# Kernel optimization log

Hardware: AMD Instinct MI355X
Metric: run time of the kernel (lower is better)

The kernel has to match this reference:

```python
import jax, jax.numpy as jnp
import numpy as np

B, S = 32, 128
NUM_Q, NUM_C = 10000, 256
DIM_K, DIM_E, DIM_CORRECT = 128, 128, 50


def setup_inputs() -> dict:
    key = jax.random.key(0)
    ks = jax.random.split(key, 16)
    w = lambda k, shape: jax.random.normal(k, shape, dtype=jnp.float32) * 0.05
    z = lambda n: jnp.zeros((n,), jnp.float32)
    # q_matrix: sparse binary concept-question map with small smoothing (typical LPKT gamma)
    q_matrix = (jax.random.uniform(ks[4], (NUM_Q + 10, NUM_C)) < 0.03).astype(jnp.float32) + 0.03
    return {
        'e_data': jax.random.randint(ks[0], (B, S), 0, NUM_Q),
        'at_data': jax.random.randint(ks[1], (B, S), 0, 3600),
        'it_data': jax.random.randint(ks[2], (B, S), 0, 43200),
        'a_data': jax.random.uniform(ks[3], (B, S), dtype=jnp.float32),
        'q_matrix': q_matrix,
        'e_E': w(ks[5], (NUM_Q + 10, DIM_K)),
        'at_E': w(ks[6], (3610, DIM_K)),
        'it_E': w(ks[7], (43210, DIM_K)),
        'W1': w(ks[8], (DIM_E + DIM_K + DIM_CORRECT, DIM_K)), 'b1': z(DIM_K),
        'W2': w(ks[9], (4 * DIM_K, DIM_K)), 'b2': z(DIM_K),
        'W3': w(ks[10], (4 * DIM_K, DIM_K)), 'b3': z(DIM_K),
        'W4': w(ks[11], (3 * DIM_K, DIM_K)), 'b4': z(DIM_K),
        'W5': w(ks[12], (DIM_E + DIM_K, DIM_K)), 'b5': z(DIM_K),
        'h0': w(ks[13], (NUM_C, DIM_K)),
    }


def reference(e_data, at_data, it_data, a_data, q_matrix, e_E, at_E, it_E,
              W1, b1, W2, b2, W3, b3, W4, b4, W5, b5, h0):
    Bn, Sn = e_data.shape
    K = W1.shape[1]
    e_emb = e_E[e_data]          # [B,S,K]
    at_emb = at_E[at_data]       # [B,S,K]
    it_emb = it_E[it_data]       # [B,S,K]
    a_rep = jnp.broadcast_to(a_data[:, :, None], (Bn, Sn, DIM_CORRECT))
    all_learning = jnp.concatenate([e_emb, at_emb, a_rep], -1) @ W1 + b1  # [B,S,K]
    q_all = q_matrix[e_data]     # [B,S,C]

    h_init = jnp.broadcast_to(h0, (Bn,) + h0.shape)              # [B,C,K]
    h_tilde_init = jnp.einsum('bc,bck->bk', q_all[:, 0], h_init)  # [B,K]
    learning_init = jnp.zeros((Bn, K), all_learning.dtype)

    xs = jax.tree.map(lambda x: jnp.swapaxes(x, 0, 1),
                      (q_all[:, :-1], q_all[:, 1:], all_learning[:, :-1],
                       it_emb[:, :-1], e_emb[:, 1:]))

    def step(carry, x):
        h, h_tilde, learning_pre = carry
        q_e, q_next, learning, it, e_next = x
        zcat = jnp.concatenate([learning_pre, it, learning, h_tilde], -1)  # [B,4K]
        lg = jnp.tanh(zcat @ W2 + b2)
        gamma_l = jax.nn.sigmoid(zcat @ W3 + b3)
        LG = gamma_l * (lg + 1.0) * 0.5                                    # [B,K]
        LG_tilde = q_e[:, :, None] * LG[:, None, :]                        # [B,C,K] (dropout=eval identity)
        gf_in = jnp.concatenate([h,
                                 jnp.broadcast_to(LG[:, None, :], h.shape),
                                 jnp.broadcast_to(it[:, None, :], h.shape)], -1)
        gamma_f = jax.nn.sigmoid(gf_in @ W4 + b4)                          # [B,C,K]
        h_new = LG_tilde + gamma_f * h
        h_tilde_new = jnp.einsum('bc,bck->bk', q_next, h_new)             # [B,K]
        y = jax.nn.sigmoid(jnp.concatenate([e_next, h_tilde_new], -1) @ W5 + b5).sum(-1) / K
        return (h_new, h_tilde_new, learning), y

    _, ys = jax.lax.scan(step, (h_init, h_tilde_init, learning_init), xs)  # ys: [S-1,B]
    pred = jnp.concatenate([jnp.zeros((Bn, 1), ys.dtype), ys.T], axis=1)    # [B,S]
    return pred
```

## Files before the change

### kernel.cpp

```cpp
#include <hip/hip_runtime.h>
#include <stdint.h>

#define S   128
#define NB  32
#define NC  256
#define DK  128
#define NSL 4
#define HROW 264

typedef __bf16 bf16x8 __attribute__((ext_vector_type(8)));
typedef float  f32x16 __attribute__((ext_vector_type(16)));
typedef unsigned int u32x4 __attribute__((ext_vector_type(4)));
typedef unsigned int u32x2 __attribute__((ext_vector_type(2)));
typedef _Float16 f16x2 __attribute__((ext_vector_type(2)));
static_assert(sizeof(bf16x8) == 16, "bf16x8 size");
static_assert(sizeof(f16x2) == 4, "f16x2 size");

#define OFF_AL   0
#define OFF_HT   OFF_AL
#define OFF_P2   524288
#define OFF_P3   1044480
#define OFF_PS   1564672
#define OFF_PY   2084864
#define OFF_WT5  2654208
#define OFF_CM   2670592

__device__ __forceinline__ float v_exp2(float x){ float r; asm("v_exp_f32 %0, %1" : "=v"(r) : "v"(x)); return r; }
__device__ __forceinline__ float v_rcp (float x){ float r; asm("v_rcp_f32 %0, %1" : "=v"(r) : "v"(x)); return r; }
__device__ __forceinline__ float sigm(float x){ return v_rcp(1.0f + v_exp2(x * -1.4426950408889634f)); }
__device__ __forceinline__ uint32_t pkbf(float lo, float hi){
  uint32_t r; asm("v_cvt_pk_bf16_f32 %0, %1, %2" : "=v"(r) : "v"(lo), "v"(hi)); return r;
}
__device__ __forceinline__ float bfhi(uint32_t w){ return __builtin_bit_cast(float, w & 0xffff0000u); }
__device__ __forceinline__ uint32_t pkh(float a, float b){
  return __builtin_bit_cast(uint32_t, __builtin_amdgcn_cvt_pkrtz(a, b));
}
__device__ __forceinline__ float fdot2u(uint32_t a, uint32_t b, float c){
  return __builtin_amdgcn_fdot2(__builtin_bit_cast(f16x2, a), __builtin_bit_cast(f16x2, b), c, false);
}
#define NLOG2E (-1.4426950408889634f)

__global__ __launch_bounds__(512) void k0_al(
    const int* __restrict__ e_data, const int* __restrict__ at_data,
    const float* __restrict__ a_data, const float* __restrict__ e_E,
    const float* __restrict__ at_E, const float* __restrict__ W1,
    const float* __restrict__ b1, float* __restrict__ ws)
{
  __shared__ float ein[32][128];
  __shared__ float atin[32][128];
  int b = blockIdx.x >> 2, q4 = blockIdx.x & 3, t0 = q4 * 32;
  for (int idx = threadIdx.x; idx < 32 * 128; idx += 512) {
    int r = idx >> 7, j = idx & 127;
    int ev  = e_data [b * S + t0 + r];
    int atv = at_data[b * S + t0 + r];
    ein [r][j] = e_E [ev  * DK + j];
    atin[r][j] = at_E[atv * DK + j];
  }
  __syncthreads();
  int j = threadIdx.x & 127, tq = threadIdx.x >> 7;
  float w1s = 0.f;
  for (int d = 0; d < 50; ++d) w1s += W1[(256 + d) * DK + j];
  float acc[8];
#pragma unroll
  for (int u = 0; u < 8; ++u) {
    int t = t0 + tq * 8 + u;
    acc[u] = b1[j] + a_data[b * S + t] * w1s;
  }
  for (int k = 0; k < 128; ++k) {
    float w = W1[k * DK + j];
#pragma unroll
    for (int u = 0; u < 8; ++u) acc[u] += ein[tq * 8 + u][k] * w;
  }
  for (int k = 0; k < 128; ++k) {
    float w = W1[(128 + k) * DK + j];
#pragma unroll
    for (int u = 0; u < 8; ++u) acc[u] += atin[tq * 8 + u][k] * w;
  }
#pragma unroll
  for (int u = 0; u < 8; ++u)
    ws[OFF_AL + (b * S + t0 + tq * 8 + u) * DK + j] = acc[u];
}

__global__ __launch_bounds__(256) void kT_tr(const float* __restrict__ W5, float* __restrict__ ws)
{
  int idx = blockIdx.x * 256 + threadIdx.x;
  int j = idx >> 7, k = idx & 127;
  ws[OFF_WT5 + j * DK + k] = W5[(128 + k) * DK + j];
}

__global__ __launch_bounds__(512) void k1_pre(
    const int* __restrict__ e_data, const int* __restrict__ it_data,
    const float* __restrict__ it_E, const float* __restrict__ e_E,
    const float* __restrict__ W2, const float* __restrict__ b2,
    const float* __restrict__ W3, const float* __restrict__ b3,
    const float* __restrict__ W4, const float* __restrict__ b4,
    const float* __restrict__ W5, const float* __restrict__ b5,
    float* __restrict__ ws)
{
  __shared__ float als[33][128];
  __shared__ float its[32][128];
  __shared__ float ens[32][128];
  int b = blockIdx.x >> 2, sh = blockIdx.x & 3, s0 = sh * 32;
  for (int idx = threadIdx.x; idx < 33 * 128; idx += 512) {
    int r = idx >> 7, j = idx & 127;
    int srow = s0 - 1 + r;
    als[r][j] = (srow >= 0) ? ws[OFF_AL + (b * S + srow) * DK + j] : 0.f;
  }
  for (int idx = threadIdx.x; idx < 32 * 128; idx += 512) {
    int r = idx >> 7, j = idx & 127;
    int itv = it_data[b * S + s0 + r];
    its[r][j] = it_E[itv * DK + j];
    int sg = s0 + r + 1; if (sg > 127) sg = 127;
    int ev = e_data[b * S + sg];
    ens[r][j] = e_E[ev * DK + j];
  }
  __syncthreads();
  int j = threadIdx.x & 127, sq = threadIdx.x >> 7;
  float p2[8], p3[8], pS[8], pY[8];
#pragma unroll
  for (int u = 0; u < 8; ++u) { p2[u] = b2[j]; p3[u] = b3[j]; pS[u] = b4[j]; pY[u] = b5[j]; }
  for (int k = 0; k < 128; ++k) {
    float w2 = W2[k * DK + j], w3 = W3[k * DK + j];
#pragma unroll
    for (int u = 0; u < 8; ++u) { float v = als[sq * 8 + u][k]; p2[u] += v * w2; p3[u] += v * w3; }
  }
  for (int k = 0; k < 128; ++k) {
    float w2 = W2[(128 + k) * DK + j], w3 = W3[(128 + k) * DK + j], w4 = W4[(256 + k) * DK + j];
#pragma unroll
    for (int u = 0; u < 8; ++u) { float v = its[sq * 8 + u][k]; p2[u] += v * w2; p3[u] += v * w3; pS[u] += v * w4; }
  }
  for (int k = 0; k < 128; ++k) {
    float w2 = W2[(256 + k) * DK + j], w3 = W3[(256 + k) * DK + j];
#pragma unroll
    for (int u = 0; u < 8; ++u) { float v = als[sq * 8 + u + 1][k]; p2[u] += v * w2; p3[u] += v * w3; }
  }
  for (int k = 0; k < 128; ++k) {
    float w5 = W5[k * DK + j];
#pragma unroll
    for (int u = 0; u < 8; ++u) pY[u] += ens[sq * 8 + u][k] * w5;
  }
#pragma unroll
  for (int u = 0; u < 8; ++u) {
    int s = s0 + sq * 8 + u;
    if (s < 127) {
      int o = (b * 127 + s) * DK + j;
      ws[OFF_P2 + o] = p2[u]; ws[OFF_P3 + o] = p3[u];
      ws[OFF_PS + o] = pS[u]; ws[OFF_PY + o] = pY[u];
    }
  }
}

__global__ __launch_bounds__(512, 2) void kmain(
    const int* __restrict__ e_data, const float* __restrict__ qmat,
    const float* __restrict__ W2, const float* __restrict__ W3,
    const float* __restrict__ W4, const float* __restrict__ h0,
    float* ws)
{
  __shared__ char     hsb[64 * HROW];
  __shared__ u32x4    W4B[4][8][64];
  __shared__ uint32_t W4Lh[64][128];
  __shared__ float    qbuf[3][64];
  __shared__ float    PST[2][3][128];
  __shared__ uint32_t htldp[64];
  __shared__ uint32_t LGp[64];

  const int bx = blockIdx.x;
  const int b = bx & 31, slice = bx >> 5;
  const int tid = threadIdx.x;
  const int lane = tid & 63, wv = tid >> 6;
  const int ct = wv >> 2, jt = wv & 3;
  const int lo = lane & 31, hi = lane >> 5;
  const int jA = tid >> 2, am = (tid >> 1) & 1, akh = tid & 1;
  const int jloc = jt * 32 + lo;

  uint32_t* cm32 = (uint32_t*)(ws + OFF_CM) + (size_t)b * 2048;

  uint32_t Awh[32];
  {
    const float* Wm = am ? W3 : W2;
#pragma unroll
    for (int i = 0; i < 32; ++i) {
      float w0 = Wm[(384 + akh * 64 + 2 * i) * DK + jA];
      float w1 = Wm[(384 + akh * 64 + 2 * i + 1) * DK + jA];
      Awh[i] = pkh(w0, w1);
    }
  }
  float hm[16];
#pragma unroll
  for (int r = 0; r < 16; ++r) {
    int cl = ct * 32 + (r & 3) + 8 * (r >> 2) + 4 * hi;
    hm[r] = h0[(slice * 64 + cl) * DK + jloc];
  }

  {
    uint32_t* w4b = (uint32_t*)&W4B[0][0][0];
#pragma unroll
    for (int it = 0; it < 16; ++it) {
      int idx = tid + it * 512;
      int w = idx & 3, l = (idx >> 2) & 63, kk = (idx >> 8) & 7, jb = idx >> 11;
      int llo = l & 31, lhi = l >> 5;
      int row = kk * 16 + lhi * 8 + 2 * w, col = jb * 32 + llo;
      w4b[idx] = pkbf(W4[row * DK + col], W4[(row + 1) * DK + col]);
    }
  }
#pragma unroll
  for (int it = 0; it < 16; ++it) {
    int idx = tid + it * 512, kp = idx >> 7, jj = idx & 127;
    W4Lh[kp][jj] = pkh(W4[(128 + 2 * kp) * DK + jj], W4[(128 + 2 * kp + 1) * DK + jj]);
  }
  if (tid < 64) {
    qbuf[0][tid] = qmat[e_data[b * S + 0] * NC + slice * 64 + tid];
    qbuf[1][tid] = qmat[e_data[b * S + 1] * NC + slice * 64 + tid];
  }
  if (tid < 384) {
    int mm = tid >> 7, jj = tid & 127;
    int off = (mm == 0) ? OFF_P2 : (mm == 1) ? OFF_P3 : OFF_PS;
    PST[0][mm][jj] = ws[off + (b * 127 + 0) * DK + jj];
  }
#pragma unroll
  for (int r = 0; r < 16; ++r) {
    int cl = ct * 32 + (r & 3) + 8 * (r >> 2) + 4 * hi;
    *(uint16_t*)(hsb + cl * HROW + jloc * 2) = (uint16_t)pkbf(hm[r], 0.f);
  }
  __syncthreads();

  {
    float ht = 0.f;
#pragma unroll
    for (int r = 0; r < 16; ++r) {
      int cl = ct * 32 + (r & 3) + 8 * (r >> 2) + 4 * hi;
      ht += qbuf[0][cl] * hm[r];
    }
    ht += __shfl_xor(ht, 32);
    if (hi == 0)
      __hip_atomic_store(&cm32[1 * 1024 + (slice * 2 + ct) * 128 + jloc],
                         pkbf(0.f, ht) | 1u, __ATOMIC_RELAXED, __HIP_MEMORY_SCOPE_AGENT);
  }

  float v0 = 0.f, v1 = 0.f;

#pragma unroll 1
  for (int s = 0; s < S - 1; ++s) {
    const int par = s & 1;

    float qld = 0.f, pld = 0.f;
    if (tid >= 448)
      qld = qmat[e_data[b * S + min(s + 2, S - 1)] * NC + slice * 64 + (tid - 448)];
    if (tid >= 128) {
      int mm = (tid - 128) >> 7, jj = tid & 127;
      int off = (mm == 0) ? OFF_P2 : (mm == 1) ? OFF_P3 : OFF_PS;
      pld = ws[off + (b * 127 + min(s + 1, 126)) * DK + jj];
    }

    f32x16 acc;
#pragma unroll
    for (int r = 0; r < 16; ++r) acc[r] = 0.f;
    {
      const char* base = hsb + (ct * 32 + lo) * HROW;
#pragma unroll
      for (int kk = 0; kk < 8; ++kk) {
        u32x2 a0 = *(const u32x2*)(base + kk * 32 + hi * 16);
        u32x2 a1 = *(const u32x2*)(base + kk * 32 + hi * 16 + 8);
        u32x4 af4; af4[0] = a0[0]; af4[1] = a0[1]; af4[2] = a1[0]; af4[3] = a1[1];
        u32x4 bfr = W4B[jt][kk][lane];
        acc = __builtin_amdgcn_mfma_f32_32x32x16_bf16(
            __builtin_bit_cast(bf16x8, af4), __builtin_bit_cast(bf16x8, bfr), acc, 0, 0, 0);
      }
    }

    if (wv == 0) {
      const uint32_t tgt = (uint32_t)(s + 1);
      const uint32_t* src = cm32 + ((s + 1) & 1) * 1024;
      uint32_t g[16];
      for (;;) {
        uint32_t tsum = 0;
#pragma unroll
        for (int i = 0; i < 16; ++i) {
          g[i] = __hip_atomic_load(&src[(i >> 1) * 128 + (i & 1) * 64 + lane],
                                   __ATOMIC_RELAXED, __HIP_MEMORY_SCOPE_AGENT);
          tsum += g[i] & 0xffffu;
        }
        if (__all(tsum == 16u * tgt)) break;
        __builtin_amdgcn_s_sleep(1);
      }
      v0 = 0.f; v1 = 0.f;
#pragma unroll
      for (int i = 0; i < 16; i += 2) { v0 += bfhi(g[i]); v1 += bfhi(g[i + 1]); }
      float vn0 = __shfl_xor(v0, 1), vn1 = __shfl_xor(v1, 1);
      if (!(lane & 1)) {
        htldp[lane >> 1]        = pkh(v0, vn0);
        htldp[32 + (lane >> 1)] = pkh(v1, vn1);
      }
    }
    __syncthreads();

    if (slice == 0 && s > 0 && wv == 0) {
      ws[OFF_HT + (b * 127 + (s - 1)) * DK + lane]      = v0;
      ws[OFF_HT + (b * 127 + (s - 1)) * DK + 64 + lane] = v1;
    }
    {
      float p = 0.f;
#pragma unroll
      for (int t = 0; t < 32; ++t)
        p = fdot2u(htldp[akh * 32 + t], Awh[t], p);
      p += __shfl_xor(p, 1);
      float po = __shfl_xor(p, 2);
      float v2 = am ? po : p;
      float v3 = am ? p : po;
      v2 += PST[par][0][jA];
      v3 += PST[par][1][jA];
      float lg = sigm(v3) * sigm(2.f * v2);
      float lgn = __shfl_xor(lg, 4);
      if ((tid & 7) == 0) LGp[tid >> 3] = pkh(lg, lgn);
    }
    __syncthreads();

    if (tid >= 448) qbuf[(s + 2) % 3][tid - 448] = qld;
    if (tid >= 128) {
      int mm = (tid - 128) >> 7, jj = tid & 127;
      PST[(s + 1) & 1][mm][jj] = pld;
    }
    {
      float pB = 0.f;
#pragma unroll
      for (int t = 0; t < 32; ++t)
        pB = fdot2u(LGp[hi * 32 + t], W4Lh[hi * 32 + t][jloc], pB);
      pB += __shfl_xor(pB, 32);
      float sb = PST[par][2][jloc] + pB;
      float sn = sb * NLOG2E;
      f16x2 l2 = __builtin_bit_cast(f16x2, LGp[jloc >> 1]);
      float lgj = (float)l2[jloc & 1];
      const float* qc = &qbuf[s % 3][0];
      const float* qn = &qbuf[(s + 1) % 3][0];
      float ht = 0.f;
#pragma unroll
      for (int q4 = 0; q4 < 4; ++q4) {
        int cbase = ct * 32 + 8 * q4 + 4 * hi;
        float4 qe4 = *(const float4*)&qc[cbase];
        float4 qn4 = *(const float4*)&qn[cbase];
#pragma unroll
        for (int rr = 0; rr < 4; ++rr) {
          int r = 4 * q4 + rr;
          float qe = (rr == 0) ? qe4.x : (rr == 1) ? qe4.y : (rr == 2) ? qe4.z : qe4.w;
          float qq = (rr == 0) ? qn4.x : (rr == 1) ? qn4.y : (rr == 2) ? qn4.z : qn4.w;
          int cl = cbase + rr;
          float g = v_rcp(1.0f + v_exp2(fmaf(acc[r], NLOG2E, sn)));
          float hn = fmaf(g, hm[r], qe * lgj);
          hm[r] = hn; ht = fmaf(qq, hn, ht);
          *(uint16_t*)(hsb + cl * HROW + jloc * 2) = (uint16_t)pkbf(hn, 0.f);
        }
      }
      ht += __shfl_xor(ht, 32);
      if (hi == 0)
        __hip_atomic_store(&cm32[(s & 1) * 1024 + (slice * 2 + ct) * 128 + jloc],
                           pkbf(0.f, ht) | (uint32_t)(s + 2),
                           __ATOMIC_RELAXED, __HIP_MEMORY_SCOPE_AGENT);
    }
    __syncthreads();
  }

  if (slice == 0 && wv == 0) {
    const uint32_t* src = cm32 + 0 * 1024;
    uint32_t g[16];
    for (;;) {
      uint32_t tsum = 0;
#pragma unroll
      for (int i = 0; i < 16; ++i) {
        g[i] = __hip_atomic_load(&src[(i >> 1) * 128 + (i & 1) * 64 + lane],
                                 __ATOMIC_RELAXED, __HIP_MEMORY_SCOPE_AGENT);
        tsum += g[i] & 0xffffu;
      }
      if (__all(tsum == 16u * 128u)) break;
      __builtin_amdgcn_s_sleep(1);
    }
    float t0 = 0.f, t1 = 0.f;
#pragma unroll
    for (int i = 0; i < 16; i += 2) { t0 += bfhi(g[i]); t1 += bfhi(g[i + 1]); }
    ws[OFF_HT + (b * 127 + 126) * DK + lane]      = t0;
    ws[OFF_HT + (b * 127 + 126) * DK + 64 + lane] = t1;
  }
}

__global__ __launch_bounds__(128) void k2_y(const float* __restrict__ ws, float* __restrict__ out)
{
  __shared__ float hts[8][128];
  __shared__ float part[2][8];
  int b = blockIdx.x >> 4, ch = blockIdx.x & 15, s0 = ch * 8;
  int j = threadIdx.x;
#pragma unroll
  for (int u = 0; u < 8; ++u) {
    int s = s0 + u;
    hts[u][j] = (s < 127) ? ws[OFF_HT + (b * 127 + s) * DK + j] : 0.f;
  }
  __syncthreads();
  float acc[8];
#pragma unroll
  for (int u = 0; u < 8; ++u) {
    int s = s0 + u;
    acc[u] = (s < 127) ? ws[OFF_PY + (b * 127 + s) * DK + j] : 0.f;
  }
  const float4* w5 = (const float4*)(ws + OFF_WT5 + j * DK);
#pragma unroll 8
  for (int i = 0; i < 32; ++i) {
    float4 w = w5[i];
#pragma unroll
    for (int u = 0; u < 8; ++u) {
      float4 h4 = *(const float4*)&hts[u][4 * i];
      acc[u] += w.x * h4.x + w.y * h4.y + w.z * h4.z + w.w * h4.w;
    }
  }
#pragma unroll
  for (int u = 0; u < 8; ++u) {
    float v = sigm(acc[u]);
#pragma unroll
    for (int off = 32; off >= 1; off >>= 1) v += __shfl_xor(v, off);
    if ((j & 63) == 0) part[j >> 6][u] = v;
  }
  __syncthreads();
  if (j < 8) {
    int s = s0 + j;
    if (s < 127) out[b * S + s + 1] = (part[0][j] + part[1][j]) * (1.0f / 128.0f);
  }
  if (j == 0 && ch == 0) out[b * S] = 0.f;
}

extern "C" void kernel_launch(void* const* d_in, const int* in_sizes, int n_in,
                              void* d_out, int out_size, void* d_ws, size_t ws_size,
                              hipStream_t stream)
{
  (void)in_sizes; (void)n_in; (void)out_size; (void)ws_size;
  const int*   e_data  = (const int*)  d_in[0];
  const int*   at_data = (const int*)  d_in[1];
  const int*   it_data = (const int*)  d_in[2];
  const float* a_data  = (const float*)d_in[3];
  const float* qmat    = (const float*)d_in[4];
  const float* e_E     = (const float*)d_in[5];
  const float* at_E    = (const float*)d_in[6];
  const float* it_E    = (const float*)d_in[7];
  const float* W1 = (const float*)d_in[8];  const float* b1 = (const float*)d_in[9];
  const float* W2 = (const float*)d_in[10]; const float* b2 = (const float*)d_in[11];
  const float* W3 = (const float*)d_in[12]; const float* b3 = (const float*)d_in[13];
  const float* W4 = (const float*)d_in[14]; const float* b4 = (const float*)d_in[15];
  const float* W5 = (const float*)d_in[16]; const float* b5 = (const float*)d_in[17];
  const float* h0 = (const float*)d_in[18];
  float* ws  = (float*)d_ws;
  float* out = (float*)d_out;

  hipMemsetAsync((char*)d_ws + (size_t)OFF_CM * 4, 0, (size_t)NB * 2 * 8 * 128 * 4, stream);

  k0_al <<<128, 512, 0, stream>>>(e_data, at_data, a_data, e_E, at_E, W1, b1, ws);
  kT_tr <<<64, 256, 0, stream>>>(W5, ws);
  k1_pre<<<128, 512, 0, stream>>>(e_data, it_data, it_E, e_E, W2, b2, W3, b3, W4, b4, W5, b5, ws);
  kmain <<<128, 512, 0, stream>>>(e_data, qmat, W2, W3, W4, h0, ws);
  k2_y  <<<512, 128, 0, stream>>>(ws, out);
}
```

Baseline: 422.1 us.

## Move cross-block h_tilde wait to loop end, split across two waves

The spin-wait on the other slices' h_tilde partials now sits at the end of each step, merged with that step's final barrier, instead of at the top of the next step. This removes one barrier per step, and two waves each poll half the columns (8 loads instead of 16). The next-step qmat and projection prefetch loads are issued one step further ahead, and the dot-product chains are split into four independent accumulators to shorten dependency latency. The cost is a longer prologue, and the wait now sits directly on the critical path between steps rather than overlapping the MFMA.

```diff
diff --git a/kernel.cpp b/kernel.cpp
--- a/kernel.cpp
+++ b/kernel.cpp
@@ -211,11 +211,13 @@
   if (tid < 64) {
     qbuf[0][tid] = qmat[e_data[b * S + 0] * NC + slice * 64 + tid];
     qbuf[1][tid] = qmat[e_data[b * S + 1] * NC + slice * 64 + tid];
+    qbuf[2][tid] = qmat[e_data[b * S + 2] * NC + slice * 64 + tid];
   }
   if (tid < 384) {
     int mm = tid >> 7, jj = tid & 127;
     int off = (mm == 0) ? OFF_P2 : (mm == 1) ? OFF_P3 : OFF_PS;
     PST[0][mm][jj] = ws[off + (b * 127 + 0) * DK + jj];
+    PST[1][mm][jj] = ws[off + (b * 127 + 1) * DK + jj];
   }
 #pragma unroll
   for (int r = 0; r < 16; ++r) {
@@ -236,21 +238,37 @@
       __hip_atomic_store(&cm32[1 * 1024 + (slice * 2 + ct) * 128 + jloc],
                          pkbf(0.f, ht) | 1u, __ATOMIC_RELAXED, __HIP_MEMORY_SCOPE_AGENT);
   }
-
-  float v0 = 0.f, v1 = 0.f;
+  float vreg = 0.f;
+  if (wv < 2) {
+    uint32_t g[8];
+    for (;;) {
+      uint32_t tsum = 0;
+#pragma unroll
+      for (int p = 0; p < 8; ++p) {
+        g[p] = __hip_atomic_load(&cm32[1 * 1024 + p * 128 + wv * 64 + lane],
+                                 __ATOMIC_RELAXED, __HIP_MEMORY_SCOPE_AGENT);
+        tsum += g[p] & 0xffffu;
+      }
+      if (__all(tsum == 8u)) break;
+      __builtin_amdgcn_s_sleep(1);
+    }
+    float v = 0.f;
+#pragma unroll
+    for (int p = 0; p < 8; ++p) v += bfhi(g[p]);
+    vreg = v;
+    float vn = __shfl_xor(v, 1);
+    if (!(lane & 1)) htldp[wv * 32 + (lane >> 1)] = pkh(v, vn);
+  }
+  __syncthreads();
+
+  float qld = 0.f, pld = 0.f;
 
 #pragma unroll 1
   for (int s = 0; s < S - 1; ++s) {
     const int par = s & 1;
 
-    float qld = 0.f, pld = 0.f;
-    if (tid >= 448)
-      qld = qmat[e_data[b * S + min(s + 2, S - 1)] * NC + slice * 64 + (tid - 448)];
-    if (tid >= 128) {
-      int mm = (tid - 128) >> 7, jj = tid & 127;
-      int off = (mm == 0) ? OFF_P2 : (mm == 1) ? OFF_P3 : OFF_PS;
-      pld = ws[off + (b * 127 + min(s + 1, 126)) * DK + jj];
-    }
+    if (slice == 0 && s > 0 && wv < 2)
+      ws[OFF_HT + (b * 127 + (s - 1)) * DK + wv * 64 + lane] = vreg;
 
     f32x16 acc;
 #pragma unroll
@@ -267,42 +285,16 @@
             __builtin_bit_cast(bf16x8, af4), __builtin_bit_cast(bf16x8, bfr), acc, 0, 0, 0);
       }
     }
-
-    if (wv == 0) {
-      const uint32_t tgt = (uint32_t)(s + 1);
-      const uint32_t* src = cm32 + ((s + 1) & 1) * 1024;
-      uint32_t g[16];
-      for (;;) {
-        uint32_t tsum = 0;
-#pragma unroll
-        for (int i = 0; i < 16; ++i) {
-          g[i] = __hip_atomic_load(&src[(i >> 1) * 128 + (i & 1) * 64 + lane],
-                                   __ATOMIC_RELAXED, __HIP_MEMORY_SCOPE_AGENT);
-          tsum += g[i] & 0xffffu;
-        }
-        if (__all(tsum == 16u * tgt)) break;
-        __builtin_amdgcn_s_sleep(1);
-      }
-      v0 = 0.f; v1 = 0.f;
-#pragma unroll
-      for (int i = 0; i < 16; i += 2) { v0 += bfhi(g[i]); v1 += bfhi(g[i + 1]); }
-      float vn0 = __shfl_xor(v0, 1), vn1 = __shfl_xor(v1, 1);
-      if (!(lane & 1)) {
-        htldp[lane >> 1]        = pkh(v0, vn0);
-        htldp[32 + (lane >> 1)] = pkh(v1, vn1);
-      }
-    }
-    __syncthreads();
-
-    if (slice == 0 && s > 0 && wv == 0) {
-      ws[OFF_HT + (b * 127 + (s - 1)) * DK + lane]      = v0;
-      ws[OFF_HT + (b * 127 + (s - 1)) * DK + 64 + lane] = v1;
-    }
     {
-      float p = 0.f;
-#pragma unroll
-      for (int t = 0; t < 32; ++t)
-        p = fdot2u(htldp[akh * 32 + t], Awh[t], p);
+      float p0 = 0.f, p1 = 0.f, p2a = 0.f, p3a = 0.f;
+#pragma unroll
+      for (int t = 0; t < 8; ++t) {
+        p0  = fdot2u(htldp[akh * 32 + 4 * t + 0], Awh[4 * t + 0], p0);
+        p1  = fdot2u(htldp[akh * 32 + 4 * t + 1], Awh[4 * t + 1], p1);
+        p2a = fdot2u(htldp[akh * 32 + 4 * t + 2], Awh[4 * t + 2], p2a);
+        p3a = fdot2u(htldp[akh * 32 + 4 * t + 3], Awh[4 * t + 3], p3a);
+      }
+      float p = (p0 + p1) + (p2a + p3a);
       p += __shfl_xor(p, 1);
       float po = __shfl_xor(p, 2);
       float v2 = am ? po : p;
@@ -315,16 +307,23 @@
     }
     __syncthreads();
 
-    if (tid >= 448) qbuf[(s + 2) % 3][tid - 448] = qld;
-    if (tid >= 128) {
-      int mm = (tid - 128) >> 7, jj = tid & 127;
-      PST[(s + 1) & 1][mm][jj] = pld;
+    if (s > 0) {
+      if (tid >= 448) qbuf[(s + 2) % 3][tid - 448] = qld;
+      if (tid >= 128) {
+        int mm = (tid - 128) >> 7;
+        PST[(s + 1) & 1][mm][tid & 127] = pld;
+      }
     }
     {
-      float pB = 0.f;
-#pragma unroll
-      for (int t = 0; t < 32; ++t)
-        pB = fdot2u(LGp[hi * 32 + t], W4Lh[hi * 32 + t][jloc], pB);
+      float q0 = 0.f, q1 = 0.f, q2 = 0.f, q3 = 0.f;
+#pragma unroll
+      for (int t = 0; t < 8; ++t) {
+        q0 = fdot2u(LGp[hi * 32 + 4 * t + 0], W4Lh[hi * 32 + 4 * t + 0][jloc], q0);
+        q1 = fdot2u(LGp[hi * 32 + 4 * t + 1], W4Lh[hi * 32 + 4 * t + 1][jloc], q1);
+        q2 = fdot2u(LGp[hi * 32 + 4 * t + 2], W4Lh[hi * 32 + 4 * t + 2][jloc], q2);
+        q3 = fdot2u(LGp[hi * 32 + 4 * t + 3], W4Lh[hi * 32 + 4 * t + 3][jloc], q3);
+      }
+      float pB = (q0 + q1) + (q2 + q3);
       pB += __shfl_xor(pB, 32);
       float sb = PST[par][2][jloc] + pB;
       float sn = sb * NLOG2E;
@@ -356,29 +355,40 @@
                            pkbf(0.f, ht) | (uint32_t)(s + 2),
                            __ATOMIC_RELAXED, __HIP_MEMORY_SCOPE_AGENT);
     }
+    if (tid >= 448)
+      qld = qmat[e_data[b * S + min(s + 3, S - 1)] * NC + slice * 64 + (tid - 448)];
+    if (tid >= 128) {
+      int mm = (tid - 128) >> 7;
+      int off = (mm == 0) ? OFF_P2 : (mm == 1) ? OFF_P3 : OFF_PS;
+      pld = ws[off + (b * 127 + min(s + 2, 126)) * DK + (tid & 127)];
+    }
+    if (wv < 2) {
+      const uint32_t tgt = (uint32_t)(s + 2);
+      const uint32_t* src = cm32 + (s & 1) * 1024;
+      uint32_t g[8];
+      for (;;) {
+        uint32_t tsum = 0;
+#pragma unroll
+        for (int p = 0; p < 8; ++p) {
+          g[p] = __hip_atomic_load(&src[p * 128 + wv * 64 + lane],
+                                   __ATOMIC_RELAXED, __HIP_MEMORY_SCOPE_AGENT);
+          tsum += g[p] & 0xffffu;
+        }
+        if (__all(tsum == 8u * tgt)) break;
+        __builtin_amdgcn_s_sleep(1);
+      }
+      float v = 0.f;
+#pragma unroll
+      for (int p = 0; p < 8; ++p) v += bfhi(g[p]);
+      vreg = v;
+      float vn = __shfl_xor(v, 1);
+      if (!(lane & 1)) htldp[wv * 32 + (lane >> 1)] = pkh(v, vn);
+    }
     __syncthreads();
   }
 
-  if (slice == 0 && wv == 0) {
-    const uint32_t* src = cm32 + 0 * 1024;
-    uint32_t g[16];
-    for (;;) {
-      uint32_t tsum = 0;
-#pragma unroll
-      for (int i = 0; i < 16; ++i) {
-        g[i] = __hip_atomic_load(&src[(i >> 1) * 128 + (i & 1) * 64 + lane],
-                                 __ATOMIC_RELAXED, __HIP_MEMORY_SCOPE_AGENT);
-        tsum += g[i] & 0xffffu;
-      }
-      if (__all(tsum == 16u * 128u)) break;
-      __builtin_amdgcn_s_sleep(1);
-    }
-    float t0 = 0.f, t1 = 0.f;
-#pragma unroll
-    for (int i = 0; i < 16; i += 2) { t0 += bfhi(g[i]); t1 += bfhi(g[i + 1]); }
-    ws[OFF_HT + (b * 127 + 126) * DK + lane]      = t0;
-    ws[OFF_HT + (b * 127 + 126) * DK + 64 + lane] = t1;
-  }
+  if (slice == 0 && wv < 2)
+    ws[OFF_HT + (b * 127 + 126) * DK + wv * 64 + lane] = vreg;
 }
 
 __global__ __launch_bounds__(128) void k2_y(const float* __restrict__ ws, float* __restrict__ out)
```

Result: slower. 479.5 us (+13.6%).
